# Optimization experiments

Hardware: AMD Instinct MI355X
Metric: run time of the kernel (lower is better)

Reference implementation:

```python
import jax, jax.numpy as jnp
import numpy as np

C = 256
CQK = C // 8  # 32


def setup_inputs() -> dict:
    key = jax.random.key(0)
    ks = jax.random.split(key, 7)
    x = jax.random.normal(ks[0], (8, C, 64, 64), dtype=jnp.float32)
    s = 1.0 / np.sqrt(C)
    Wq = jax.random.normal(ks[1], (CQK, C), dtype=jnp.float32) * s
    bq = jnp.zeros((CQK,), dtype=jnp.float32)
    Wk = jax.random.normal(ks[2], (CQK, C), dtype=jnp.float32) * s
    bk = jnp.zeros((CQK,), dtype=jnp.float32)
    Wv = jax.random.normal(ks[3], (C, C), dtype=jnp.float32) * s
    bv = jnp.zeros((C,), dtype=jnp.float32)
    gamma = jnp.zeros((1,), dtype=jnp.float32)
    return {"x": x, "Wq": Wq, "bq": bq, "Wk": Wk, "bk": bk, "Wv": Wv, "bv": bv, "gamma": gamma}


def reference(x, Wq, bq, Wk, bk, Wv, bv, gamma):
    B, Cc, H, W = x.shape
    N = H * W
    xf = x.reshape(B, Cc, N)  # [B, C, N]
    # 1x1 convs == channel matmuls
    q = jnp.einsum('oc,bcn->bon', Wq, xf) + bq[None, :, None]  # [B, C//8, N]
    k = jnp.einsum('oc,bcn->bon', Wk, xf) + bk[None, :, None]  # [B, C//8, N]
    v = jnp.einsum('oc,bcn->bon', Wv, xf) + bv[None, :, None]  # [B, C, N]
    scale = float(Cc // 8) ** (-0.5)
    # attention[b, i, j] over keys j (softmax on last dim)
    scores = jnp.einsum('bon,bom->bnm', q, k) * scale  # [B, N, N]
    attn = jax.nn.softmax(scores, axis=-1)
    # out[b,c,i] = sum_j v[b,c,j] * attn[b,i,j]
    out = jnp.einsum('bcj,bij->bci', v, attn).reshape(B, Cc, H, W)
    return gamma * out + x
```

## Files before the change

### kernel.cpp

```cpp
#include <hip/hip_runtime.h>
#include <hip/hip_bf16.h>
#include <math.h>

#define B_   8
#define C_   256
#define N_   4096
#define QSCALE_L2E 0.2550541451582815f
#define DEFER_THR  11.5f

typedef __attribute__((ext_vector_type(8))) short bf16x8;
typedef __attribute__((ext_vector_type(4))) float f32x4;

__device__ __forceinline__ unsigned short bfu(float f) {
    __hip_bfloat16 h = __float2bfloat16(f);
    return __builtin_bit_cast(unsigned short, h);
}
__device__ __forceinline__ unsigned cvtpk(float lo, float hi) {
    unsigned r;
    asm("v_cvt_pk_bf16_f32 %0, %1, %2" : "=v"(r) : "v"(lo), "v"(hi));
    return r;
}

__global__ __launch_bounds__(256) void w_prep(
    const float* __restrict__ Wq, const float* __restrict__ Wk,
    const float* __restrict__ Wv, unsigned short* __restrict__ wbf)
{
    const int i = blockIdx.x * 256 + threadIdx.x;
    const int off = i * 4;
    float4 f;
    if (off < 32 * C_)            f = *reinterpret_cast<const float4*>(Wq + off);
    else if (off < 64 * C_)       f = *reinterpret_cast<const float4*>(Wk + off - 32 * C_);
    else                          f = *reinterpret_cast<const float4*>(Wv + off - 64 * C_);
    ushort4 u;
    u.x = bfu(f.x); u.y = bfu(f.y); u.z = bfu(f.z); u.w = bfu(f.w);
    *reinterpret_cast<ushort4*>(wbf + off) = u;
}

__global__ __launch_bounds__(256, 2) void qkv_proj_mfma(
    const float* __restrict__ x, const unsigned short* __restrict__ wbf,
    const float* __restrict__ bq, const float* __restrict__ bk,
    const float* __restrict__ bv,
    unsigned short* __restrict__ q, unsigned short* __restrict__ k,
    unsigned short* __restrict__ v)
{
    const int b = blockIdx.y, n0 = blockIdx.x * 64;
    const int t = threadIdx.x;
    const int w = t >> 6, l = t & 63;
    const int li = l & 15, g = l >> 4;

    __shared__ unsigned short xT[64 * 256];
    __shared__ unsigned short qkS[2 * 64 * 32];

    {
        const int n = t & 63;
        const int cq0 = t >> 6;
        const float* xb = x + ((size_t)b * C_) * N_ + n0 + n;
        #pragma unroll 4
        for (int s = 0; s < 16; ++s) {
            const int cq = cq0 + 4 * s;
            const float f0 = xb[(size_t)(cq * 4 + 0) * N_];
            const float f1 = xb[(size_t)(cq * 4 + 1) * N_];
            const float f2 = xb[(size_t)(cq * 4 + 2) * N_];
            const float f3 = xb[(size_t)(cq * 4 + 3) * N_];
            ushort4 pk;
            pk.x = bfu(f0); pk.y = bfu(f1); pk.z = bfu(f2); pk.w = bfu(f3);
            const int byte = n * 512 + (((cq >> 1) ^ (n & 7)) << 4) + (cq & 1) * 8;
            *reinterpret_cast<ushort4*>(reinterpret_cast<char*>(xT) + byte) = pk;
        }
    }
    __syncthreads();

    const unsigned short* wq_bf = wbf;
    const unsigned short* wk_bf = wbf + 32 * C_;
    const unsigned short* wv_bf = wbf + 64 * C_;

    const unsigned short* wqk_bf = (w < 2) ? wq_bf : wk_bf;
    const float* bqk = (w < 2) ? bq : bk;
    const float qscl = (w < 2) ? QSCALE_L2E : 1.0f;
    const int mt0 = (w & 1) * 2;
    const int ov0 = w * 64;

    f32x4 accv[4][4];
    f32x4 accq[2][2];
    const f32x4 z4 = {0.f, 0.f, 0.f, 0.f};
    #pragma unroll
    for (int a = 0; a < 4; ++a)
        #pragma unroll
        for (int c2 = 0; c2 < 4; ++c2) accv[a][c2] = z4;
    #pragma unroll
    for (int a = 0; a < 2; ++a)
        #pragma unroll
        for (int c2 = 0; c2 < 2; ++c2) accq[a][c2] = z4;

    #pragma unroll 2
    for (int kk = 0; kk < 8; ++kk) {
        bf16x8 xf[4];
        #pragma unroll
        for (int nt = 0; nt < 4; ++nt) {
            const int row = nt * 16 + li;
            const int byte = row * 512 + (((kk * 4 + g) ^ (row & 7)) << 4);
            xf[nt] = *reinterpret_cast<const bf16x8*>(
                reinterpret_cast<const char*>(xT) + byte);
        }
        #pragma unroll
        for (int ot = 0; ot < 4; ++ot) {
            const bf16x8 wV = *reinterpret_cast<const bf16x8*>(
                wv_bf + (size_t)(ov0 + ot * 16 + li) * C_ + kk * 32 + g * 8);
            #pragma unroll
            for (int nt = 0; nt < 4; ++nt)
                accv[nt][ot] = __builtin_amdgcn_mfma_f32_16x16x32_bf16(
                    xf[nt], wV, accv[nt][ot], 0, 0, 0);
        }
        #pragma unroll
        for (int ot = 0; ot < 2; ++ot) {
            const bf16x8 wA = *reinterpret_cast<const bf16x8*>(
                wqk_bf + (size_t)(ot * 16 + li) * C_ + kk * 32 + g * 8);
            #pragma unroll
            for (int m2 = 0; m2 < 2; ++m2)
                accq[ot][m2] = __builtin_amdgcn_mfma_f32_16x16x32_bf16(
                    wA, xf[mt0 + m2], accq[ot][m2], 0, 0, 0);
        }
    }

    __syncthreads();

    {
        const int qk = (w < 2) ? 0 : 1;
        #pragma unroll
        for (int ot = 0; ot < 2; ++ot) {
            const int d0 = ot * 16 + 4 * g;
            const float4 b4 = *reinterpret_cast<const float4*>(bqk + d0);
            const int slot = ot * 4 + g;
            #pragma unroll
            for (int m2 = 0; m2 < 2; ++m2) {
                const int n = (mt0 + m2) * 16 + li;
                ushort4 s4;
                s4.x = bfu((accq[ot][m2][0] + b4.x) * qscl);
                s4.y = bfu((accq[ot][m2][1] + b4.y) * qscl);
                s4.z = bfu((accq[ot][m2][2] + b4.z) * qscl);
                s4.w = bfu((accq[ot][m2][3] + b4.w) * qscl);
                const int byte = qk * 4096 + n * 64 + ((slot ^ (n & 7)) << 3);
                *reinterpret_cast<ushort4*>(reinterpret_cast<char*>(qkS) + byte) = s4;
            }
        }
    }
    {
        #pragma unroll
        for (int ot = 0; ot < 4; ++ot) {
            const int o = ov0 + ot * 16 + li;
            const float bias = bv[o];
            #pragma unroll
            for (int nt = 0; nt < 4; ++nt) {
                ushort4 s4;
                s4.x = bfu(accv[nt][ot][0] + bias);
                s4.y = bfu(accv[nt][ot][1] + bias);
                s4.z = bfu(accv[nt][ot][2] + bias);
                s4.w = bfu(accv[nt][ot][3] + bias);
                const int slot = nt * 4 + g;
                const int byte = o * 128 + ((slot ^ (o & 7)) << 3);
                *reinterpret_cast<ushort4*>(reinterpret_cast<char*>(xT) + byte) = s4;
            }
        }
    }
    __syncthreads();

    {
        const char* qks = reinterpret_cast<const char*>(qkS);
        #pragma unroll
        for (int qk = 0; qk < 2; ++qk) {
            const int n = t >> 2, s2 = (t & 3) * 2;
            const int byteA = qk * 4096 + n * 64 + (((s2    ) ^ (n & 7)) << 3);
            const int byteB = qk * 4096 + n * 64 + (((s2 + 1) ^ (n & 7)) << 3);
            const uint2 lo = *reinterpret_cast<const uint2*>(qks + byteA);
            const uint2 hi = *reinterpret_cast<const uint2*>(qks + byteB);
            uint4 val = make_uint4(lo.x, lo.y, hi.x, hi.y);
            unsigned short* dst = (qk == 0) ? q : k;
            *reinterpret_cast<uint4*>(dst + ((size_t)b * N_ + n0) * 32 + t * 8) = val;
        }
    }
    {
        const char* vs = reinterpret_cast<const char*>(xT);
        #pragma unroll
        for (int p2 = 0; p2 < 8; ++p2) {
            const int o = p2 * 32 + (t >> 3);
            const int s2 = (t & 7) * 2;
            const int byteA = o * 128 + (((s2    ) ^ (o & 7)) << 3);
            const int byteB = o * 128 + (((s2 + 1) ^ (o & 7)) << 3);
            const uint2 lo = *reinterpret_cast<const uint2*>(vs + byteA);
            const uint2 hi = *reinterpret_cast<const uint2*>(vs + byteB);
            uint4 val = make_uint4(lo.x, lo.y, hi.x, hi.y);
            *reinterpret_cast<uint4*>(v + ((size_t)b * C_ + o) * N_ + n0 + (t & 7) * 8) = val;
        }
    }
}

__global__ __launch_bounds__(512, 2) void attn_mfma(
    const unsigned short* __restrict__ q, const unsigned short* __restrict__ k,
    const unsigned short* __restrict__ v,
    const float* __restrict__ x, const float* __restrict__ gamma,
    float* __restrict__ out)
{
    const int id = blockIdx.x;
    const int b = id & 7;
    const int i0 = (id >> 3) * 128;
    const int t = threadIdx.x;
    const int w = t >> 6, l = t & 63;
    const int li = l & 15, g = l >> 4;
    const int QS = w & 3;
    const int JH = w >> 2;

    __shared__ unsigned short kT[2][128 * 32];
    __shared__ __align__(16) unsigned short vT[2][2][256 * 64];
    __shared__ float m_x[4][2][2][16];
    __shared__ float l_x[4][2][2][16];

    const unsigned short* qb = q + (size_t)b * N_ * 32;
    const unsigned short* kb = k + (size_t)b * N_ * 32;
    const unsigned short* vb = v + ((size_t)b * C_) * N_;

    const bf16x8 qfA = *reinterpret_cast<const bf16x8*>(
        qb + (size_t)(i0 + QS * 32 + li) * 32 + g * 8);
    const bf16x8 qfB = *reinterpret_cast<const bf16x8*>(
        qb + (size_t)(i0 + QS * 32 + 16 + li) * 32 + g * 8);

    f32x4 accA[16], accB[16];
    const f32x4 z4 = {0.f, 0.f, 0.f, 0.f};
    #pragma unroll
    for (int a = 0; a < 16; ++a) { accA[a] = z4; accB[a] = z4; }

    float m_runA = -3.0e38f, m_runB = -3.0e38f;
    float l_pA = 0.f, l_pB = 0.f;

    const int tt = t & 255, hh = t >> 8;
    const int jr = tt >> 2, sl = tt & 3;
    const int jt_s = jr >> 4, gg = (jr >> 2) & 3, rr = jr & 3;
    const int jloc = (jt_s >> 1) * 32 + (jt_s & 1) * 4 + gg * 8 + rr;
    const int s_src = sl ^ (jr & 3);
    const int koff_sh = (hh * 64 + jloc) * 32 + s_src * 8;
    const unsigned voffK = (unsigned)(koff_sh * 2);
    const int kdst_off = hh * 2048 + tt * 8;

    const int sIdx = t >> 8;
    const int w4 = (t >> 6) & 3;
    const int vrow0 = w4 * 16 + (l >> 2);
    const int vchunk = l & 3;
    unsigned voffVb[4];
    int vdst[4][2];
    #pragma unroll
    for (int p = 0; p < 4; ++p) {
        const int row = vrow0 + p * 64;
        voffVb[p] = (unsigned)(((size_t)row * N_ + sIdx * 64 + vchunk * 16) * 2);
        const int s0 = vchunk * 2;
        vdst[p][0] = row * 128 + (((s0    ) ^ (row & 7)) << 4);
        vdst[p][1] = row * 128 + (((s0 + 1) ^ (row & 7)) << 4);
    }

    union PB { unsigned wo[4]; bf16x8 v8; };

    {
        const bf16x8 k0 = *reinterpret_cast<const bf16x8*>(
            reinterpret_cast<const char*>(kb) + voffK);
        *reinterpret_cast<bf16x8*>(&kT[0][kdst_off]) = k0;
        #pragma unroll
        for (int p = 0; p < 4; ++p) {
            const char* src = reinterpret_cast<const char*>(vb) + voffVb[p];
            const bf16x8 a0 = *reinterpret_cast<const bf16x8*>(src);
            const bf16x8 a1 = *reinterpret_cast<const bf16x8*>(src + 16);
            char* vd = reinterpret_cast<char*>(&vT[0][sIdx][0]);
            *reinterpret_cast<bf16x8*>(vd + vdst[p][0]) = a0;
            *reinterpret_cast<bf16x8*>(vd + vdst[p][1]) = a1;
        }
    }
    __syncthreads();

    for (int jj = 0; jj < 32; ++jj) {
        const int cur = jj & 1, nxt = cur ^ 1;
        const bool pf = (jj + 1 < 32);

        bf16x8 knx;
        bf16x8 vnx[4][2];
        if (pf) {
            const unsigned short* sbk = kb + (size_t)(jj + 1) * 128 * 32;
            asm volatile("global_load_dwordx4 %0, %1, %2"
                         : "=v"(knx) : "v"(voffK), "s"(sbk));
            const unsigned short* sbv = vb + (size_t)(jj + 1) * 128;
            #pragma unroll
            for (int p = 0; p < 4; ++p)
                asm volatile("global_load_dwordx4 %0, %2, %3\n\t"
                             "global_load_dwordx4 %1, %2, %3 offset:16"
                             : "=v"(vnx[p][0]), "=v"(vnx[p][1])
                             : "v"(voffVb[p]), "s"(sbv));
            __builtin_amdgcn_sched_barrier(0);
        }

        f32x4 sTA[4], sTB[4];
        {
            const char* kbuf = reinterpret_cast<const char*>(&kT[cur][0]) + JH * 4096;
            #pragma unroll
            for (int jt = 0; jt < 4; ++jt) {
                const int row = jt * 16 + li;
                const bf16x8 kA = *reinterpret_cast<const bf16x8*>(
                    kbuf + row * 64 + ((g ^ (row & 3)) << 4));
                sTA[jt] = __builtin_amdgcn_mfma_f32_16x16x32_bf16(kA, qfA, z4, 0, 0, 0);
                sTB[jt] = __builtin_amdgcn_mfma_f32_16x16x32_bf16(kA, qfB, z4, 0, 0, 0);
            }
        }

        float mxA = fmaxf(fmaxf(fmaxf(sTA[0][0], sTA[0][1]), fmaxf(sTA[0][2], sTA[0][3])),
                          fmaxf(fmaxf(sTA[1][0], sTA[1][1]), fmaxf(sTA[1][2], sTA[1][3])));
        mxA = fmaxf(mxA, fmaxf(fmaxf(fmaxf(sTA[2][0], sTA[2][1]), fmaxf(sTA[2][2], sTA[2][3])),
                               fmaxf(fmaxf(sTA[3][0], sTA[3][1]), fmaxf(sTA[3][2], sTA[3][3]))));
        float mxB = fmaxf(fmaxf(fmaxf(sTB[0][0], sTB[0][1]), fmaxf(sTB[0][2], sTB[0][3])),
                          fmaxf(fmaxf(sTB[1][0], sTB[1][1]), fmaxf(sTB[1][2], sTB[1][3])));
        mxB = fmaxf(mxB, fmaxf(fmaxf(fmaxf(sTB[2][0], sTB[2][1]), fmaxf(sTB[2][2], sTB[2][3])),
                               fmaxf(fmaxf(sTB[3][0], sTB[3][1]), fmaxf(sTB[3][2], sTB[3][3]))));
        if (__any(fmaxf(mxA - m_runA, mxB - m_runB) > DEFER_THR)) {
            float mwA = fmaxf(mxA, __shfl_xor(mxA, 16));
            mwA = fmaxf(mwA, __shfl_xor(mwA, 32));
            float mwB = fmaxf(mxB, __shfl_xor(mxB, 16));
            mwB = fmaxf(mwB, __shfl_xor(mwB, 32));
            const float mnA = fmaxf(m_runA, mwA);
            const float mnB = fmaxf(m_runB, mwB);
            const float fA = __builtin_amdgcn_exp2f(m_runA - mnA);
            const float fB = __builtin_amdgcn_exp2f(m_runB - mnB);
            m_runA = mnA; m_runB = mnB;
            l_pA *= fA;   l_pB *= fB;
            #pragma unroll
            for (int ct = 0; ct < 16; ++ct) { accA[ct] *= fA; accB[ct] *= fB; }
        }
        #pragma unroll
        for (int jt = 0; jt < 4; ++jt)
            #pragma unroll
            for (int r = 0; r < 4; ++r) {
                sTA[jt][r] = __builtin_amdgcn_exp2f(sTA[jt][r] - m_runA);
                sTB[jt][r] = __builtin_amdgcn_exp2f(sTB[jt][r] - m_runB);
            }
        {
            const f32x4 svA = (sTA[0] + sTA[1]) + (sTA[2] + sTA[3]);
            const f32x4 svB = (sTB[0] + sTB[1]) + (sTB[2] + sTB[3]);
            l_pA += (svA[0] + svA[1]) + (svA[2] + svA[3]);
            l_pB += (svB[0] + svB[1]) + (svB[2] + svB[3]);
        }

        PB pbA0, pbA1, pbB0, pbB1;
        pbA0.wo[0] = cvtpk(sTA[0][0], sTA[0][1]); pbA0.wo[1] = cvtpk(sTA[0][2], sTA[0][3]);
        pbA0.wo[2] = cvtpk(sTA[1][0], sTA[1][1]); pbA0.wo[3] = cvtpk(sTA[1][2], sTA[1][3]);
        pbA1.wo[0] = cvtpk(sTA[2][0], sTA[2][1]); pbA1.wo[1] = cvtpk(sTA[2][2], sTA[2][3]);
        pbA1.wo[2] = cvtpk(sTA[3][0], sTA[3][1]); pbA1.wo[3] = cvtpk(sTA[3][2], sTA[3][3]);
        pbB0.wo[0] = cvtpk(sTB[0][0], sTB[0][1]); pbB0.wo[1] = cvtpk(sTB[0][2], sTB[0][3]);
        pbB0.wo[2] = cvtpk(sTB[1][0], sTB[1][1]); pbB0.wo[3] = cvtpk(sTB[1][2], sTB[1][3]);
        pbB1.wo[0] = cvtpk(sTB[2][0], sTB[2][1]); pbB1.wo[1] = cvtpk(sTB[2][2], sTB[2][3]);
        pbB1.wo[2] = cvtpk(sTB[3][0], sTB[3][1]); pbB1.wo[3] = cvtpk(sTB[3][2], sTB[3][3]);

        __builtin_amdgcn_s_setprio(1);
        {
            const char* vbuf = reinterpret_cast<const char*>(&vT[cur][JH][0]);
            #pragma unroll
            for (int ct = 0; ct < 16; ++ct) {
                const int vrow = ct * 16 + li;
                const bf16x8 vA0 = *reinterpret_cast<const bf16x8*>(
                    vbuf + vrow * 128 + (((g    ) ^ (vrow & 7)) << 4));
                const bf16x8 vA1 = *reinterpret_cast<const bf16x8*>(
                    vbuf + vrow * 128 + (((4 + g) ^ (vrow & 7)) << 4));
                accA[ct] = __builtin_amdgcn_mfma_f32_16x16x32_bf16(vA0, pbA0.v8, accA[ct], 0, 0, 0);
                accB[ct] = __builtin_amdgcn_mfma_f32_16x16x32_bf16(vA0, pbB0.v8, accB[ct], 0, 0, 0);
                accA[ct] = __builtin_amdgcn_mfma_f32_16x16x32_bf16(vA1, pbA1.v8, accA[ct], 0, 0, 0);
                accB[ct] = __builtin_amdgcn_mfma_f32_16x16x32_bf16(vA1, pbB1.v8, accB[ct], 0, 0, 0);
            }
        }
        __builtin_amdgcn_s_setprio(0);

        if (pf) {
            asm volatile("s_waitcnt vmcnt(0)" ::: "memory");
            __builtin_amdgcn_sched_barrier(0);
            *reinterpret_cast<bf16x8*>(&kT[nxt][kdst_off]) = knx;
            char* vd = reinterpret_cast<char*>(&vT[nxt][sIdx][0]);
            #pragma unroll
            for (int p = 0; p < 4; ++p) {
                *reinterpret_cast<bf16x8*>(vd + vdst[p][0]) = vnx[p][0];
                *reinterpret_cast<bf16x8*>(vd + vdst[p][1]) = vnx[p][1];
            }
        }
        __syncthreads();
    }

    float lA = l_pA, lB = l_pB;
    lA += __shfl_xor(lA, 16); lA += __shfl_xor(lA, 32);
    lB += __shfl_xor(lB, 16); lB += __shfl_xor(lB, 32);

    if (l < 16) {
        m_x[QS][JH][0][li] = m_runA; m_x[QS][JH][1][li] = m_runB;
        l_x[QS][JH][0][li] = lA;     l_x[QS][JH][1][li] = lB;
    }

    f32x4* mrg = reinterpret_cast<f32x4*>(&vT[0][0][0]);
    if (JH == 0) {
        #pragma unroll
        for (int c8 = 0; c8 < 8; ++c8) {
            mrg[((((QS * 2 + 0) * 2 + 0) * 8 + c8) << 6) + l] = accA[8 + c8];
            mrg[((((QS * 2 + 0) * 2 + 1) * 8 + c8) << 6) + l] = accB[8 + c8];
        }
    } else {
        #pragma unroll
        for (int c8 = 0; c8 < 8; ++c8) {
            mrg[((((QS * 2 + 1) * 2 + 0) * 8 + c8) << 6) + l] = accA[c8];
            mrg[((((QS * 2 + 1) * 2 + 1) * 8 + c8) << 6) + l] = accB[c8];
        }
    }
    __syncthreads();

    const int PJ = JH ^ 1;
    const float mpA = m_x[QS][PJ][0][li], mpB = m_x[QS][PJ][1][li];
    const float lqA = l_x[QS][PJ][0][li], lqB = l_x[QS][PJ][1][li];
    const float mMA = fmaxf(m_runA, mpA);
    const float mMB = fmaxf(m_runB, mpB);
    const float fsA = __builtin_amdgcn_exp2f(m_runA - mMA);
    const float fpA = __builtin_amdgcn_exp2f(mpA - mMA);
    const float fsB = __builtin_amdgcn_exp2f(m_runB - mMB);
    const float fpB = __builtin_amdgcn_exp2f(mpB - mMB);
    const float linvA = 1.0f / (lA * fsA + lqA * fpA);
    const float linvB = 1.0f / (lB * fsB + lqB * fpB);

    const float gm = gamma[0];
    const int iA = i0 + QS * 32 + li;
    const float* xb2 = x + ((size_t)b * C_) * N_;
    float* ob = out + ((size_t)b * C_) * N_;
    if (JH == 0) {
        #pragma unroll
        for (int c8 = 0; c8 < 8; ++c8) {
            const f32x4 oA = accA[c8] * fsA
                + mrg[((((QS * 2 + 1) * 2 + 0) * 8 + c8) << 6) + l] * fpA;
            const f32x4 oB = accB[c8] * fsB
                + mrg[((((QS * 2 + 1) * 2 + 1) * 8 + c8) << 6) + l] * fpB;
            #pragma unroll
            for (int r = 0; r < 4; ++r) {
                const int c = c8 * 16 + 4 * g + r;
                const size_t off = (size_t)c * N_ + iA;
                ob[off]      = gm * oA[r] * linvA + xb2[off];
                ob[off + 16] = gm * oB[r] * linvB + xb2[off + 16];
            }
        }
    } else {
        #pragma unroll
        for (int c8 = 0; c8 < 8; ++c8) {
            const f32x4 oA = accA[8 + c8] * fsA
                + mrg[((((QS * 2 + 0) * 2 + 0) * 8 + c8) << 6) + l] * fpA;
            const f32x4 oB = accB[8 + c8] * fsB
                + mrg[((((QS * 2 + 0) * 2 + 1) * 8 + c8) << 6) + l] * fpB;
            #pragma unroll
            for (int r = 0; r < 4; ++r) {
                const int c = (8 + c8) * 16 + 4 * g + r;
                const size_t off = (size_t)c * N_ + iA;
                ob[off]      = gm * oA[r] * linvA + xb2[off];
                ob[off + 16] = gm * oB[r] * linvB + xb2[off + 16];
            }
        }
    }
}

extern "C" void kernel_launch(void* const* d_in, const int* in_sizes, int n_in,
                              void* d_out, int out_size, void* d_ws, size_t ws_size,
                              hipStream_t stream) {
    const float* x     = (const float*)d_in[0];
    const float* Wq    = (const float*)d_in[1];
    const float* bq    = (const float*)d_in[2];
    const float* Wk    = (const float*)d_in[3];
    const float* bk    = (const float*)d_in[4];
    const float* Wv    = (const float*)d_in[5];
    const float* bv    = (const float*)d_in[6];
    const float* gamma = (const float*)d_in[7];
    float* out = (float*)d_out;

    unsigned short* q   = (unsigned short*)d_ws;
    unsigned short* k   = q + (size_t)B_ * N_ * 32;
    unsigned short* v   = k + (size_t)B_ * N_ * 32;
    unsigned short* wbf = v + (size_t)B_ * C_ * N_;

    dim3 grid(N_ / 64, B_);
    w_prep<<<80, 256, 0, stream>>>(Wq, Wk, Wv, wbf);
    qkv_proj_mfma<<<grid, 256, 0, stream>>>(x, wbf, bq, bk, bv, q, k, v);
    attn_mfma<<<256, 512, 0, stream>>>(q, k, v, x, gamma, out);
}
```

Baseline: 135.1 us.

## Software-pipeline QK of next tile with PV of previous tile

Restructures the attention main loop so each iteration computes QK scores for the current K/V tile while running the PV accumulation MFMAs for the previous tile, whose packed probabilities are carried in registers. A prologue handles the first tile's QK and softmax and an epilogue does the final PV. The aim is to let the independent QK and PV MFMAs and the softmax exp work overlap instead of sitting in one serial chain. In exchange it adds an extra __syncthreads per iteration, keeps more live registers, and uses a different offset expression for the first K load.

After: 137.6 us. Within noise of the previous version (+1.8%).

```diff
diff --git a/kernel.cpp b/kernel.cpp
--- a/kernel.cpp
+++ b/kernel.cpp
@@ -256,56 +256,48 @@
     }
 
     union PB { unsigned wo[4]; bf16x8 v8; };
-
-    {
-        const bf16x8 k0 = *reinterpret_cast<const bf16x8*>(
-            reinterpret_cast<const char*>(kb) + voffK);
-        *reinterpret_cast<bf16x8*>(&kT[0][kdst_off]) = k0;
+    struct Pq { bf16x8 f0, f1, f2, f3; };
+    Pq pa;
+
+    bf16x8 knx;
+    bf16x8 vnx[4][2];
+
+    auto vissue = [&](int tile) {
+        const unsigned short* sbk = kb + (size_t)tile * 128 * 32;
+        asm volatile("global_load_dwordx4 %0, %1, %2"
+                     : "=v"(knx) : "v"(voffK), "s"(sbk));
+        const unsigned short* sbv = vb + (size_t)tile * 128;
+        #pragma unroll
+        for (int p = 0; p < 4; ++p)
+            asm volatile("global_load_dwordx4 %0, %2, %3\n\t"
+                         "global_load_dwordx4 %1, %2, %3 offset:16"
+                         : "=v"(vnx[p][0]), "=v"(vnx[p][1])
+                         : "v"(voffVb[p]), "s"(sbv));
+        __builtin_amdgcn_sched_barrier(0);
+    };
+    auto vwrite = [&](int nb) {
+        asm volatile("s_waitcnt vmcnt(0)" ::: "memory");
+        __builtin_amdgcn_sched_barrier(0);
+        *reinterpret_cast<bf16x8*>(&kT[nb][kdst_off]) = knx;
+        char* vd = reinterpret_cast<char*>(&vT[nb][sIdx][0]);
         #pragma unroll
         for (int p = 0; p < 4; ++p) {
-            const char* src = reinterpret_cast<const char*>(vb) + voffVb[p];
-            const bf16x8 a0 = *reinterpret_cast<const bf16x8*>(src);
-            const bf16x8 a1 = *reinterpret_cast<const bf16x8*>(src + 16);
-            char* vd = reinterpret_cast<char*>(&vT[0][sIdx][0]);
-            *reinterpret_cast<bf16x8*>(vd + vdst[p][0]) = a0;
-            *reinterpret_cast<bf16x8*>(vd + vdst[p][1]) = a1;
-        }
-    }
-    __syncthreads();
-
-    for (int jj = 0; jj < 32; ++jj) {
-        const int cur = jj & 1, nxt = cur ^ 1;
-        const bool pf = (jj + 1 < 32);
-
-        bf16x8 knx;
-        bf16x8 vnx[4][2];
-        if (pf) {
-            const unsigned short* sbk = kb + (size_t)(jj + 1) * 128 * 32;
-            asm volatile("global_load_dwordx4 %0, %1, %2"
-                         : "=v"(knx) : "v"(voffK), "s"(sbk));
-            const unsigned short* sbv = vb + (size_t)(jj + 1) * 128;
-            #pragma unroll
-            for (int p = 0; p < 4; ++p)
-                asm volatile("global_load_dwordx4 %0, %2, %3\n\t"
-                             "global_load_dwordx4 %1, %2, %3 offset:16"
-                             : "=v"(vnx[p][0]), "=v"(vnx[p][1])
-                             : "v"(voffVb[p]), "s"(sbv));
-            __builtin_amdgcn_sched_barrier(0);
-        }
-
-        f32x4 sTA[4], sTB[4];
-        {
-            const char* kbuf = reinterpret_cast<const char*>(&kT[cur][0]) + JH * 4096;
-            #pragma unroll
-            for (int jt = 0; jt < 4; ++jt) {
-                const int row = jt * 16 + li;
-                const bf16x8 kA = *reinterpret_cast<const bf16x8*>(
-                    kbuf + row * 64 + ((g ^ (row & 3)) << 4));
-                sTA[jt] = __builtin_amdgcn_mfma_f32_16x16x32_bf16(kA, qfA, z4, 0, 0, 0);
-                sTB[jt] = __builtin_amdgcn_mfma_f32_16x16x32_bf16(kA, qfB, z4, 0, 0, 0);
-            }
-        }
-
+            *reinterpret_cast<bf16x8*>(vd + vdst[p][0]) = vnx[p][0];
+            *reinterpret_cast<bf16x8*>(vd + vdst[p][1]) = vnx[p][1];
+        }
+    };
+    auto qk8 = [&](int cur, f32x4* sTA, f32x4* sTB) {
+        const char* kbuf = reinterpret_cast<const char*>(&kT[cur][0]) + JH * 4096;
+        #pragma unroll
+        for (int jt = 0; jt < 4; ++jt) {
+            const int row = jt * 16 + li;
+            const bf16x8 kA = *reinterpret_cast<const bf16x8*>(
+                kbuf + row * 64 + ((g ^ (row & 3)) << 4));
+            sTA[jt] = __builtin_amdgcn_mfma_f32_16x16x32_bf16(kA, qfA, z4, 0, 0, 0);
+            sTB[jt] = __builtin_amdgcn_mfma_f32_16x16x32_bf16(kA, qfB, z4, 0, 0, 0);
+        }
+    };
+    auto smpack = [&](f32x4* sTA, f32x4* sTB) {
         float mxA = fmaxf(fmaxf(fmaxf(sTA[0][0], sTA[0][1]), fmaxf(sTA[0][2], sTA[0][3])),
                           fmaxf(fmaxf(sTA[1][0], sTA[1][1]), fmaxf(sTA[1][2], sTA[1][3])));
         mxA = fmaxf(mxA, fmaxf(fmaxf(fmaxf(sTA[2][0], sTA[2][1]), fmaxf(sTA[2][2], sTA[2][3])),
@@ -335,54 +327,79 @@
                 sTA[jt][r] = __builtin_amdgcn_exp2f(sTA[jt][r] - m_runA);
                 sTB[jt][r] = __builtin_amdgcn_exp2f(sTB[jt][r] - m_runB);
             }
-        {
-            const f32x4 svA = (sTA[0] + sTA[1]) + (sTA[2] + sTA[3]);
-            const f32x4 svB = (sTB[0] + sTB[1]) + (sTB[2] + sTB[3]);
-            l_pA += (svA[0] + svA[1]) + (svA[2] + svA[3]);
-            l_pB += (svB[0] + svB[1]) + (svB[2] + svB[3]);
-        }
-
-        PB pbA0, pbA1, pbB0, pbB1;
-        pbA0.wo[0] = cvtpk(sTA[0][0], sTA[0][1]); pbA0.wo[1] = cvtpk(sTA[0][2], sTA[0][3]);
-        pbA0.wo[2] = cvtpk(sTA[1][0], sTA[1][1]); pbA0.wo[3] = cvtpk(sTA[1][2], sTA[1][3]);
-        pbA1.wo[0] = cvtpk(sTA[2][0], sTA[2][1]); pbA1.wo[1] = cvtpk(sTA[2][2], sTA[2][3]);
-        pbA1.wo[2] = cvtpk(sTA[3][0], sTA[3][1]); pbA1.wo[3] = cvtpk(sTA[3][2], sTA[3][3]);
-        pbB0.wo[0] = cvtpk(sTB[0][0], sTB[0][1]); pbB0.wo[1] = cvtpk(sTB[0][2], sTB[0][3]);
-        pbB0.wo[2] = cvtpk(sTB[1][0], sTB[1][1]); pbB0.wo[3] = cvtpk(sTB[1][2], sTB[1][3]);
-        pbB1.wo[0] = cvtpk(sTB[2][0], sTB[2][1]); pbB1.wo[1] = cvtpk(sTB[2][2], sTB[2][3]);
-        pbB1.wo[2] = cvtpk(sTB[3][0], sTB[3][1]); pbB1.wo[3] = cvtpk(sTB[3][2], sTB[3][3]);
-
+        const f32x4 svA = (sTA[0] + sTA[1]) + (sTA[2] + sTA[3]);
+        const f32x4 svB = (sTB[0] + sTB[1]) + (sTB[2] + sTB[3]);
+        l_pA += (svA[0] + svA[1]) + (svA[2] + svA[3]);
+        l_pB += (svB[0] + svB[1]) + (svB[2] + svB[3]);
+        PB a0, a1, b0, b1;
+        a0.wo[0] = cvtpk(sTA[0][0], sTA[0][1]); a0.wo[1] = cvtpk(sTA[0][2], sTA[0][3]);
+        a0.wo[2] = cvtpk(sTA[1][0], sTA[1][1]); a0.wo[3] = cvtpk(sTA[1][2], sTA[1][3]);
+        a1.wo[0] = cvtpk(sTA[2][0], sTA[2][1]); a1.wo[1] = cvtpk(sTA[2][2], sTA[2][3]);
+        a1.wo[2] = cvtpk(sTA[3][0], sTA[3][1]); a1.wo[3] = cvtpk(sTA[3][2], sTA[3][3]);
+        b0.wo[0] = cvtpk(sTB[0][0], sTB[0][1]); b0.wo[1] = cvtpk(sTB[0][2], sTB[0][3]);
+        b0.wo[2] = cvtpk(sTB[1][0], sTB[1][1]); b0.wo[3] = cvtpk(sTB[1][2], sTB[1][3]);
+        b1.wo[0] = cvtpk(sTB[2][0], sTB[2][1]); b1.wo[1] = cvtpk(sTB[2][2], sTB[2][3]);
+        b1.wo[2] = cvtpk(sTB[3][0], sTB[3][1]); b1.wo[3] = cvtpk(sTB[3][2], sTB[3][3]);
+        pa.f0 = a0.v8; pa.f1 = a1.v8; pa.f2 = b0.v8; pa.f3 = b1.v8;
+    };
+    auto pv64 = [&](int cur) {
         __builtin_amdgcn_s_setprio(1);
-        {
-            const char* vbuf = reinterpret_cast<const char*>(&vT[cur][JH][0]);
-            #pragma unroll
-            for (int ct = 0; ct < 16; ++ct) {
-                const int vrow = ct * 16 + li;
-                const bf16x8 vA0 = *reinterpret_cast<const bf16x8*>(
-                    vbuf + vrow * 128 + (((g    ) ^ (vrow & 7)) << 4));
-                const bf16x8 vA1 = *reinterpret_cast<const bf16x8*>(
-                    vbuf + vrow * 128 + (((4 + g) ^ (vrow & 7)) << 4));
-                accA[ct] = __builtin_amdgcn_mfma_f32_16x16x32_bf16(vA0, pbA0.v8, accA[ct], 0, 0, 0);
-                accB[ct] = __builtin_amdgcn_mfma_f32_16x16x32_bf16(vA0, pbB0.v8, accB[ct], 0, 0, 0);
-                accA[ct] = __builtin_amdgcn_mfma_f32_16x16x32_bf16(vA1, pbA1.v8, accA[ct], 0, 0, 0);
-                accB[ct] = __builtin_amdgcn_mfma_f32_16x16x32_bf16(vA1, pbB1.v8, accB[ct], 0, 0, 0);
-            }
+        const char* vbuf = reinterpret_cast<const char*>(&vT[cur][JH][0]);
+        #pragma unroll
+        for (int ct = 0; ct < 16; ++ct) {
+            const int vrow = ct * 16 + li;
+            const bf16x8 vA0 = *reinterpret_cast<const bf16x8*>(
+                vbuf + vrow * 128 + (((g    ) ^ (vrow & 7)) << 4));
+            const bf16x8 vA1 = *reinterpret_cast<const bf16x8*>(
+                vbuf + vrow * 128 + (((4 + g) ^ (vrow & 7)) << 4));
+            accA[ct] = __builtin_amdgcn_mfma_f32_16x16x32_bf16(vA0, pa.f0, accA[ct], 0, 0, 0);
+            accB[ct] = __builtin_amdgcn_mfma_f32_16x16x32_bf16(vA0, pa.f2, accB[ct], 0, 0, 0);
+            accA[ct] = __builtin_amdgcn_mfma_f32_16x16x32_bf16(vA1, pa.f1, accA[ct], 0, 0, 0);
+            accB[ct] = __builtin_amdgcn_mfma_f32_16x16x32_bf16(vA1, pa.f3, accB[ct], 0, 0, 0);
         }
         __builtin_amdgcn_s_setprio(0);
-
-        if (pf) {
-            asm volatile("s_waitcnt vmcnt(0)" ::: "memory");
-            __builtin_amdgcn_sched_barrier(0);
-            *reinterpret_cast<bf16x8*>(&kT[nxt][kdst_off]) = knx;
-            char* vd = reinterpret_cast<char*>(&vT[nxt][sIdx][0]);
-            #pragma unroll
-            for (int p = 0; p < 4; ++p) {
-                *reinterpret_cast<bf16x8*>(vd + vdst[p][0]) = vnx[p][0];
-                *reinterpret_cast<bf16x8*>(vd + vdst[p][1]) = vnx[p][1];
-            }
-        }
+    };
+
+    {
+        const bf16x8 k0 = *reinterpret_cast<const bf16x8*>(
+            reinterpret_cast<const char*>(kb) + (size_t)koff_sh * 2);
+        *reinterpret_cast<bf16x8*>(&kT[0][kdst_off]) = k0;
+        #pragma unroll
+        for (int p = 0; p < 4; ++p) {
+            const char* src = reinterpret_cast<const char*>(vb) + voffVb[p];
+            const bf16x8 a0 = *reinterpret_cast<const bf16x8*>(src);
+            const bf16x8 a1 = *reinterpret_cast<const bf16x8*>(src + 16);
+            char* vd = reinterpret_cast<char*>(&vT[0][sIdx][0]);
+            *reinterpret_cast<bf16x8*>(vd + vdst[p][0]) = a0;
+            *reinterpret_cast<bf16x8*>(vd + vdst[p][1]) = a1;
+        }
+    }
+    __syncthreads();
+
+    f32x4 sTA[4], sTB[4];
+    {
+        vissue(1);
+        qk8(0, sTA, sTB);
+        smpack(sTA, sTB);
+        vwrite(1);
+    }
+    __syncthreads();
+
+    for (int jj = 1; jj < 32; ++jj) {
+        const int cur = jj & 1, prv = cur ^ 1;
+        const bool pf = (jj + 1 < 32);
+
+        if (pf) vissue(jj + 1);
+        qk8(cur, sTA, sTB);
+        pv64(prv);
+        smpack(sTA, sTB);
         __syncthreads();
-    }
+        if (pf) vwrite(prv);
+        __syncthreads();
+    }
+
+    pv64(1);
+    __syncthreads();
 
     float lA = l_pA, lB = l_pB;
     lA += __shfl_xor(lA, 16); lA += __shfl_xor(lA, 32);
```
